# Performance work log

Hardware: AMD Instinct MI355X
Metric: run time of the kernel (lower is better)

The kernel has to match this reference:

```python
import jax, jax.numpy as jnp
import numpy as np

B, IC, HW = 16, 32, 128
NF, OC, K, GROUP = 8, 64, 5, 8


def _rotate_filters(w, theta):
    """Bilinear rotation of filters w [N, C, k, k] by angle theta.
    Matches torch affine_grid + grid_sample (align_corners=False, zero padding)."""
    k = w.shape[-1]
    base = (2.0 * jnp.arange(k, dtype=w.dtype) + 1.0) / k - 1.0  # pixel-center normalized coords
    ys, xs = jnp.meshgrid(base, base, indexing='ij')  # [k, k]
    c, s = jnp.cos(theta), jnp.sin(theta)
    # sampling grid = rot_mat @ [x, y, 1]
    gx = c * xs - s * ys
    gy = s * xs + c * ys
    # normalized -> pixel coords (align_corners=False)
    ix = ((gx + 1.0) * k - 1.0) / 2.0
    iy = ((gy + 1.0) * k - 1.0) / 2.0
    x0 = jnp.floor(ix)
    y0 = jnp.floor(iy)
    wx1 = ix - x0
    wy1 = iy - y0
    wx0 = 1.0 - wx1
    wy0 = 1.0 - wy1

    def gather(yy, xx):
        valid = ((xx >= 0) & (xx < k) & (yy >= 0) & (yy < k)).astype(w.dtype)
        xc = jnp.clip(xx, 0, k - 1).astype(jnp.int32)
        yc = jnp.clip(yy, 0, k - 1).astype(jnp.int32)
        return w[:, :, yc, xc] * valid  # [N, C, k, k]

    return (gather(y0, x0) * (wy0 * wx0)
            + gather(y0, x0 + 1.0) * (wy0 * wx1)
            + gather(y0 + 1.0, x0) * (wy1 * wx0)
            + gather(y0 + 1.0, x0 + 1.0) * (wy1 * wx1))


def _forward(x, kernel, relaxed_weights):
    nf, oc, ic, k, _ = kernel.shape
    group = relaxed_weights.shape[1]
    wflat = kernel.reshape(nf * oc, ic, k, k)
    thetas = -2.0 * jnp.pi / group * jnp.arange(group, dtype=x.dtype)
    # [group, nf*oc, ic, k, k]
    fb = jax.vmap(lambda t: _rotate_filters(wflat, t))(thetas)
    # -> [nf, oc, group, ic, k, k]
    fb = jnp.transpose(fb, (1, 0, 2, 3, 4)).reshape(nf, oc, group, ic, k, k)
    w = jnp.einsum('na,noaikl->oaikl', relaxed_weights, fb)
    w = w.reshape(oc * group, ic, k, k)
    pad = (k - 1) // 2
    y = jax.lax.conv_general_dilated(
        x, w, window_strides=(1, 1), padding=[(pad, pad), (pad, pad)],
        dimension_numbers=('NCHW', 'OIHW', 'NCHW'))
    b, _, h, wd = y.shape
    y = y.reshape(b, oc, group, wd, h)  # matches torch .view(B, O, A, W, H)
    return jax.nn.leaky_relu(y, negative_slope=0.01)


def setup_inputs() -> dict:
    key = jax.random.key(0)
    k1, k2, k3 = jax.random.split(key, 3)
    x = jax.random.normal(k1, (B, IC, HW, HW), dtype=jnp.float32)
    kernel = jax.random.normal(k2, (NF, OC, IC, K, K), dtype=jnp.float32) * 0.05
    relaxed_weights = jax.random.normal(k3, (NF, GROUP), dtype=jnp.float32)
    return {"x": x, "kernel": kernel, "relaxed_weights": relaxed_weights}


def reference(x, kernel, relaxed_weights):
    return _forward(x, kernel, relaxed_weights)
```

## Files before the change

### kernel.cpp

```cpp
#include <hip/hip_runtime.h>
#include <hip/hip_bf16.h>
#include <math.h>

#define B_   16
#define IC_  32
#define HW_  128
#define NF_  8
#define OC_  64
#define K_   5
#define GRP_ 8
#define COTOT_ (OC_ * GRP_)
#define XTH  132
#define TAPSTRIDE (COTOT_ * IC_)

typedef short  short8  __attribute__((ext_vector_type(8)));
typedef unsigned short ushort8 __attribute__((ext_vector_type(8)));
typedef float  f32x4   __attribute__((ext_vector_type(4)));

static __device__ inline unsigned short f2bf(float f) {
    unsigned u = __builtin_bit_cast(unsigned, f);
    unsigned r = (u + 0x7FFFu + ((u >> 16) & 1u)) >> 16;
    return (unsigned short)r;
}

__device__ __forceinline__ void gload16(void* lds, const void* g) {
    __builtin_amdgcn_global_load_lds(
        (const __attribute__((address_space(1))) unsigned int*)g,
        (__attribute__((address_space(3))) unsigned int*)lds, 16, 0, 0);
}

__global__ __launch_bounds__(256) void xform_kernel(
    const float* __restrict__ x, unsigned short* __restrict__ xt) {
    int idx = blockIdx.x * blockDim.x + threadIdx.x;
    const int TOT = B_ * XTH * XTH;
    if (idx >= TOT) return;
    int wp = idx % XTH;
    int t  = idx / XTH;
    int hp = t % XTH;
    int b  = t / XTH;

    unsigned short vals[IC_];
    bool interior = (hp >= 2) && (hp < 2 + HW_) && (wp >= 2) && (wp < 2 + HW_);
    if (interior) {
        const float* xb = x + ((size_t)b * IC_) * (HW_ * HW_) + (hp - 2) * HW_ + (wp - 2);
        #pragma unroll
        for (int ic = 0; ic < IC_; ++ic)
            vals[ic] = f2bf(xb[(size_t)ic * (HW_ * HW_)]);
    } else {
        #pragma unroll
        for (int ic = 0; ic < IC_; ++ic) vals[ic] = 0;
    }
    ushort8* dst = (ushort8*)(xt + (size_t)idx * IC_);
    #pragma unroll
    for (int c = 0; c < 4; ++c) {
        ushort8 v;
        #pragma unroll
        for (int j = 0; j < 8; ++j) v[j] = vals[c * 8 + j];
        dst[c] = v;
    }
}

__global__ __launch_bounds__(256) void build_w_kernel(
    const float* __restrict__ kern,
    const float* __restrict__ relaxed,
    unsigned short* __restrict__ wt) {
    int idx = blockIdx.x * blockDim.x + threadIdx.x;
    const int TOT = 25 * COTOT_ * IC_;
    if (idx >= TOT) return;
    int ic = idx & (IC_ - 1);
    int t  = idx >> 5;
    int co = t & (COTOT_ - 1);
    int e  = t >> 9;
    int a  = co & (GRP_ - 1);
    int o  = co >> 3;
    int i  = e / K_;
    int j  = e - i * K_;

    float theta = -6.283185307179586f / (float)GRP_ * (float)a;
    float cth = cosf(theta), sth = sinf(theta);
    float bx = (2.0f * (float)j + 1.0f) / (float)K_ - 1.0f;
    float by = (2.0f * (float)i + 1.0f) / (float)K_ - 1.0f;
    float gx = cth * bx - sth * by;
    float gy = sth * bx + cth * by;
    float ix = ((gx + 1.0f) * (float)K_ - 1.0f) * 0.5f;
    float iy = ((gy + 1.0f) * (float)K_ - 1.0f) * 0.5f;
    float x0 = floorf(ix), y0 = floorf(iy);
    float wx1 = ix - x0, wy1 = iy - y0;
    float wx0 = 1.0f - wx1, wy0 = 1.0f - wy1;

    float xs2[2]  = {x0, x0 + 1.0f};
    float ys2[2]  = {y0, y0 + 1.0f};
    float wxs[2] = {wx0, wx1};
    float wys[2] = {wy0, wy1};

    float tw[4];
    int   tyc[4], txc[4];
    #pragma unroll
    for (int dy = 0; dy < 2; ++dy) {
        #pragma unroll
        for (int dx = 0; dx < 2; ++dx) {
            float xx = xs2[dx], yy = ys2[dy];
            bool valid = (xx >= 0.0f) && (xx < (float)K_) &&
                         (yy >= 0.0f) && (yy < (float)K_);
            int tp = dy * 2 + dx;
            tw[tp]  = wys[dy] * wxs[dx] * (valid ? 1.0f : 0.0f);
            txc[tp] = (int)fminf(fmaxf(xx, 0.0f), (float)(K_ - 1));
            tyc[tp] = (int)fminf(fmaxf(yy, 0.0f), (float)(K_ - 1));
        }
    }

    float acc = 0.0f;
    #pragma unroll
    for (int n = 0; n < NF_; ++n) {
        const float* kb = kern + ((size_t)((n * OC_ + o) * IC_ + ic)) * (K_ * K_);
        float v = 0.0f;
        #pragma unroll
        for (int tp = 0; tp < 4; ++tp)
            v += kb[tyc[tp] * K_ + txc[tp]] * tw[tp];
        acc += relaxed[n * GRP_ + a] * v;
    }
    wt[idx] = f2bf(acc);
}

__global__ __launch_bounds__(256, 2) void conv_mfma_kernel(
    const unsigned short* __restrict__ xt,
    const unsigned short* __restrict__ wt,
    float* __restrict__ out) {
    __shared__ __align__(16) unsigned short xs[6 * XTH * IC_];

    int tid  = threadIdx.x;
    int lane = tid & 63;
    int wv   = tid >> 6;
    int l15  = lane & 15;
    int l4   = lane >> 4;
    int hr   = wv >> 1;
    int wn   = wv & 1;

    int hp = blockIdx.x;
    int b  = blockIdx.y;
    int cg = blockIdx.z;
    int cobase = cg * 128;
    int h0 = hp * 2;

    {
        const unsigned short* xb = xt + (((size_t)b * XTH + h0) * XTH) * IC_;
        #pragma unroll
        for (int i = 0; i < 13; ++i) {
            int s = i * 256 + tid;
            if (s < 3168) gload16(&xs[s * 8], xb + (size_t)s * 8);
        }
    }

    const unsigned short* wl = wt + (size_t)(cobase + l15) * IC_ + l4 * 8;

    short8 afA[8], afB[8];
    #pragma unroll
    for (int m = 0; m < 8; ++m)
        afA[m] = *(const short8*)(wl + (size_t)m * 16 * IC_);

    f32x4 acc[8][4];
    #pragma unroll
    for (int m = 0; m < 8; ++m)
        #pragma unroll
        for (int n = 0; n < 4; ++n) acc[m][n] = (f32x4)(0.0f);

    __syncthreads();

    const char* xsb = (const char*)xs;
    int xoff = (hr * XTH + wn * 64 + l15) * 64 + l4 * 16;
    int kx = 0;

    #pragma unroll 1
    for (int pi = 0; pi < 12; ++pi) {
        int t0 = pi * 2;
        {
            const unsigned short* wp = wl + (size_t)(t0 + 1) * TAPSTRIDE;
            #pragma unroll
            for (int m = 0; m < 8; ++m)
                afB[m] = *(const short8*)(wp + (size_t)m * 16 * IC_);
        }
        {
            short8 bf[4];
            #pragma unroll
            for (int n = 0; n < 4; ++n)
                bf[n] = *(const short8*)(xsb + xoff + n * 1024);
            __builtin_amdgcn_s_setprio(1);
            #pragma unroll
            for (int m = 0; m < 8; ++m)
                #pragma unroll
                for (int n = 0; n < 4; ++n)
                    acc[m][n] = __builtin_amdgcn_mfma_f32_16x16x32_bf16(
                        afA[m], bf[n], acc[m][n], 0, 0, 0);
            __builtin_amdgcn_s_setprio(0);
        }
        if (++kx == 5) { kx = 0; xoff += 8192; } else { xoff += 64; }

        {
            const unsigned short* wp = wl + (size_t)(t0 + 2) * TAPSTRIDE;
            #pragma unroll
            for (int m = 0; m < 8; ++m)
                afA[m] = *(const short8*)(wp + (size_t)m * 16 * IC_);
        }
        {
            short8 bf[4];
            #pragma unroll
            for (int n = 0; n < 4; ++n)
                bf[n] = *(const short8*)(xsb + xoff + n * 1024);
            __builtin_amdgcn_s_setprio(1);
            #pragma unroll
            for (int m = 0; m < 8; ++m)
                #pragma unroll
                for (int n = 0; n < 4; ++n)
                    acc[m][n] = __builtin_amdgcn_mfma_f32_16x16x32_bf16(
                        afB[m], bf[n], acc[m][n], 0, 0, 0);
            __builtin_amdgcn_s_setprio(0);
        }
        if (++kx == 5) { kx = 0; xoff += 8192; } else { xoff += 64; }
    }
    {
        short8 bf[4];
        #pragma unroll
        for (int n = 0; n < 4; ++n)
            bf[n] = *(const short8*)(xsb + xoff + n * 1024);
        __builtin_amdgcn_s_setprio(1);
        #pragma unroll
        for (int m = 0; m < 8; ++m)
            #pragma unroll
            for (int n = 0; n < 4; ++n)
                acc[m][n] = __builtin_amdgcn_mfma_f32_16x16x32_bf16(
                    afA[m], bf[n], acc[m][n], 0, 0, 0);
        __builtin_amdgcn_s_setprio(0);
    }

    int h = h0 + hr;
    float* ob = out + ((size_t)b * COTOT_ + cobase) * (HW_ * HW_)
                    + (size_t)h * HW_ + wn * 64;
    #pragma unroll
    for (int m = 0; m < 8; ++m) {
        #pragma unroll
        for (int n = 0; n < 4; ++n) {
            #pragma unroll
            for (int r = 0; r < 4; ++r) {
                int co = m * 16 + l4 * 4 + r;
                int w  = n * 16 + l15;
                float v = acc[m][n][r];
                v = (v >= 0.0f) ? v : 0.01f * v;
                ob[(size_t)co * (HW_ * HW_) + w] = v;
            }
        }
    }
}

extern "C" void kernel_launch(void* const* d_in, const int* in_sizes, int n_in,
                              void* d_out, int out_size, void* d_ws, size_t ws_size,
                              hipStream_t stream) {
    const float* x       = (const float*)d_in[0];
    const float* kernel  = (const float*)d_in[1];
    const float* relaxed = (const float*)d_in[2];
    float* out = (float*)d_out;

    unsigned short* xt = (unsigned short*)d_ws;
    unsigned short* wt = (unsigned short*)((char*)d_ws + (size_t)B_ * XTH * XTH * IC_ * 2);

    const int xtot = B_ * XTH * XTH;
    xform_kernel<<<(xtot + 255) / 256, 256, 0, stream>>>(x, xt);

    const int wtot = 25 * COTOT_ * IC_;
    build_w_kernel<<<(wtot + 255) / 256, 256, 0, stream>>>(kernel, relaxed, wt);

    dim3 grid(HW_ / 2, B_, COTOT_ / 128);
    conv_mfma_kernel<<<grid, 256, 0, stream>>>(xt, wt, out);
}
```

Before: 275.0 us.

## Stage weight taps through a triple-buffered LDS ring with XOR-swizzled layouts

Weights are no longer read from global memory straight into registers, double-buffered per wave. Each tap's weight slice is now loaded asynchronously into a 3-slot shared-memory ring, two taps ahead, using vmcnt waits and barriers. Both the input tile and the weight slices use XOR-swizzled 16-byte chunks to reduce LDS bank conflicts on the MFMA operand reads. The cost is extra LDS use (24KB), two barriers per tap, and index arithmetic, which may lower occupancy or add sync stalls.

```diff
diff --git a/kernel.cpp b/kernel.cpp
--- a/kernel.cpp
+++ b/kernel.cpp
@@ -127,6 +127,7 @@
     const unsigned short* __restrict__ wt,
     float* __restrict__ out) {
     __shared__ __align__(16) unsigned short xs[6 * XTH * IC_];
+    __shared__ __align__(16) unsigned short wring[3][4096];
 
     int tid  = threadIdx.x;
     int lane = tid & 63;
@@ -147,89 +148,123 @@
         #pragma unroll
         for (int i = 0; i < 13; ++i) {
             int s = i * 256 + tid;
-            if (s < 3168) gload16(&xs[s * 8], xb + (size_t)s * 8);
-        }
-    }
-
-    const unsigned short* wl = wt + (size_t)(cobase + l15) * IC_ + l4 * 8;
-
-    short8 afA[8], afB[8];
+            if (s < 3168) {
+                int row = s / 528;
+                int rem = s - row * 528;
+                int w   = rem >> 2;
+                int p   = rem & 3;
+                int c   = p ^ ((w >> 1) & 3);
+                gload16(&xs[s * 8], xb + row * 4224 + w * 32 + c * 8);
+            }
+        }
+    }
+    {
+        const unsigned short* w0 = wt + (size_t)cobase * IC_;
+        #pragma unroll
+        for (int i = 0; i < 2; ++i) {
+            int s  = i * 256 + tid;
+            int co = s >> 2;
+            int c  = (s & 3) ^ ((s >> 3) & 3);
+            gload16(&wring[0][s * 8], w0 + (size_t)co * IC_ + c * 8);
+        }
+        const unsigned short* w1 = wt + (size_t)TAPSTRIDE + cobase * IC_;
+        #pragma unroll
+        for (int i = 0; i < 2; ++i) {
+            int s  = i * 256 + tid;
+            int co = s >> 2;
+            int c  = (s & 3) ^ ((s >> 3) & 3);
+            gload16(&wring[1][s * 8], w1 + (size_t)co * IC_ + c * 8);
+        }
+    }
+
+    f32x4 acc[8][4];
     #pragma unroll
     for (int m = 0; m < 8; ++m)
-        afA[m] = *(const short8*)(wl + (size_t)m * 16 * IC_);
-
-    f32x4 acc[8][4];
-    #pragma unroll
-    for (int m = 0; m < 8; ++m)
         #pragma unroll
         for (int n = 0; n < 4; ++n) acc[m][n] = (f32x4)(0.0f);
 
-    __syncthreads();
+    asm volatile("s_waitcnt vmcnt(2)" ::: "memory");
+    __builtin_amdgcn_s_barrier();
 
     const char* xsb = (const char*)xs;
-    int xoff = (hr * XTH + wn * 64 + l15) * 64 + l4 * 16;
+    const int awz = (l4 ^ ((l15 & 7) >> 1)) << 4;
+    int rowoff = hr * 8448;
     int kx = 0;
+    int rcur = 0;
+    int rst  = 2;
 
     #pragma unroll 1
-    for (int pi = 0; pi < 12; ++pi) {
-        int t0 = pi * 2;
+    for (int t = 0; t < 23; ++t) {
         {
-            const unsigned short* wp = wl + (size_t)(t0 + 1) * TAPSTRIDE;
+            const unsigned short* ws = wt + (size_t)(t + 2) * TAPSTRIDE + cobase * IC_;
+            #pragma unroll
+            for (int i = 0; i < 2; ++i) {
+                int s  = i * 256 + tid;
+                int co = s >> 2;
+                int c  = (s & 3) ^ ((s >> 3) & 3);
+                gload16(&wring[rst][s * 8], ws + (size_t)co * IC_ + c * 8);
+            }
+        }
+        asm volatile("s_waitcnt vmcnt(4)" ::: "memory");
+        __builtin_amdgcn_s_barrier();
+
+        {
+            const char* wb = (const char*)wring[rcur];
+            short8 af[8];
             #pragma unroll
             for (int m = 0; m < 8; ++m)
-                afB[m] = *(const short8*)(wp + (size_t)m * 16 * IC_);
-        }
-        {
+                af[m] = *(const short8*)(wb + (m * 16 + l15) * 64 + awz);
+            int base = rowoff + (wn * 64 + kx + l15) * 64 +
+                       ((l4 ^ (((kx + l15) & 7) >> 1)) << 4);
             short8 bf[4];
             #pragma unroll
             for (int n = 0; n < 4; ++n)
-                bf[n] = *(const short8*)(xsb + xoff + n * 1024);
+                bf[n] = *(const short8*)(xsb + base + n * 1024);
             __builtin_amdgcn_s_setprio(1);
             #pragma unroll
             for (int m = 0; m < 8; ++m)
                 #pragma unroll
                 for (int n = 0; n < 4; ++n)
                     acc[m][n] = __builtin_amdgcn_mfma_f32_16x16x32_bf16(
-                        afA[m], bf[n], acc[m][n], 0, 0, 0);
+                        af[m], bf[n], acc[m][n], 0, 0, 0);
             __builtin_amdgcn_s_setprio(0);
         }
-        if (++kx == 5) { kx = 0; xoff += 8192; } else { xoff += 64; }
-
+        __builtin_amdgcn_s_barrier();
+
+        if (++kx == 5) { kx = 0; rowoff += 8448; }
+        if (++rcur == 3) rcur = 0;
+        if (++rst == 3) rst = 0;
+    }
+
+    #pragma unroll 1
+    for (int t = 23; t < 25; ++t) {
+        if (t == 23) asm volatile("s_waitcnt vmcnt(2)" ::: "memory");
+        else         asm volatile("s_waitcnt vmcnt(0)" ::: "memory");
+        __builtin_amdgcn_s_barrier();
         {
-            const unsigned short* wp = wl + (size_t)(t0 + 2) * TAPSTRIDE;
+            const char* wb = (const char*)wring[rcur];
+            short8 af[8];
             #pragma unroll
             for (int m = 0; m < 8; ++m)
-                afA[m] = *(const short8*)(wp + (size_t)m * 16 * IC_);
-        }
-        {
+                af[m] = *(const short8*)(wb + (m * 16 + l15) * 64 + awz);
+            int base = rowoff + (wn * 64 + kx + l15) * 64 +
+                       ((l4 ^ (((kx + l15) & 7) >> 1)) << 4);
             short8 bf[4];
             #pragma unroll
             for (int n = 0; n < 4; ++n)
-                bf[n] = *(const short8*)(xsb + xoff + n * 1024);
+                bf[n] = *(const short8*)(xsb + base + n * 1024);
             __builtin_amdgcn_s_setprio(1);
             #pragma unroll
             for (int m = 0; m < 8; ++m)
                 #pragma unroll
                 for (int n = 0; n < 4; ++n)
                     acc[m][n] = __builtin_amdgcn_mfma_f32_16x16x32_bf16(
-                        afB[m], bf[n], acc[m][n], 0, 0, 0);
+                        af[m], bf[n], acc[m][n], 0, 0, 0);
             __builtin_amdgcn_s_setprio(0);
         }
-        if (++kx == 5) { kx = 0; xoff += 8192; } else { xoff += 64; }
-    }
-    {
-        short8 bf[4];
-        #pragma unroll
-        for (int n = 0; n < 4; ++n)
-            bf[n] = *(const short8*)(xsb + xoff + n * 1024);
-        __builtin_amdgcn_s_setprio(1);
-        #pragma unroll
-        for (int m = 0; m < 8; ++m)
-            #pragma unroll
-            for (int n = 0; n < 4; ++n)
-                acc[m][n] = __builtin_amdgcn_mfma_f32_16x16x32_bf16(
-                    afA[m], bf[n], acc[m][n], 0, 0, 0);
-        __builtin_amdgcn_s_setprio(0);
+        __builtin_amdgcn_s_barrier();
+        if (++kx == 5) { kx = 0; rowoff += 8448; }
+        if (++rcur == 3) rcur = 0;
     }
 
     int h = h0 + hr;
```

Measured after the change: 279.4 us. No clear change (+1.6%).
